# Kernel tuning notes

Measured on AMD Instinct MI355X. Metric: run time of the kernel, lower is better.

Reference implementation:

```python
import jax, jax.numpy as jnp
import numpy as np

B, NQ, NK = 4, 2048, 2048
D_MODEL, D_K, D_V, H = 1024, 1024, 1024, 16


def setup_inputs() -> dict:
    key = jax.random.key(0)
    ks = jax.random.split(key, 8)
    return {
        "queries": jax.random.normal(ks[0], (B, NQ, D_MODEL), dtype=jnp.float32),
        "keys": jax.random.normal(ks[1], (B, NK, D_MODEL), dtype=jnp.float32),
        "values": jax.random.normal(ks[2], (B, NK, D_MODEL), dtype=jnp.float32),
        # nn.Linear weights init.normal_(std=0.001); stored here in (in, out) layout
        "Wq": jax.random.normal(ks[3], (D_MODEL, D_K), dtype=jnp.float32) * 0.001,
        "Wk": jax.random.normal(ks[4], (D_MODEL, D_K), dtype=jnp.float32) * 0.001,
        "Wv": jax.random.normal(ks[5], (D_MODEL, D_V), dtype=jnp.float32) * 0.001,
        "Wo": jax.random.normal(ks[6], (D_V, D_MODEL), dtype=jnp.float32) * 0.001,
        "bo": jnp.zeros((D_MODEL,), dtype=jnp.float32),
    }


def reference(queries, keys, values, Wq, Wk, Wv, Wo, bo):
    b_s, nq, _ = queries.shape
    nk = keys.shape[1]
    hd_k = D_K // H  # per-head key dim
    hd_v = D_V // H  # per-head value dim
    # projections -> [b, h, n, hd]
    q = (queries @ Wq).reshape(b_s, nq, H, hd_k).transpose(0, 2, 1, 3)
    k = (keys @ Wk).reshape(b_s, nk, H, hd_k).transpose(0, 2, 1, 3)
    v = (values @ Wv).reshape(b_s, nk, H, hd_v).transpose(0, 2, 1, 3)
    # NOTE: original scales by sqrt(d_k) (full d_k), not per-head dim
    att = jnp.einsum("bhqd,bhkd->bhqk", q, k) / np.float32(np.sqrt(D_K))
    att = jax.nn.softmax(att, axis=-1)
    # dropout = identity (eval mode)
    out = jnp.einsum("bhqk,bhkd->bhqd", att, v)
    out = out.transpose(0, 2, 1, 3).reshape(b_s, nq, D_V)
    return out @ Wo + bo
```

## Files before the change

kernel.cpp:

```cpp
#include <hip/hip_runtime.h>


#define DM    1024
#define NSEQ  2048
#define HEADS 16
#define HD    64

typedef float floatx4 __attribute__((ext_vector_type(4)));
typedef short s16x4   __attribute__((ext_vector_type(4)));
typedef short s16x8   __attribute__((ext_vector_type(8)));
typedef unsigned int u32x4 __attribute__((ext_vector_type(4)));

static __device__ __forceinline__ floatx4 mfma_bf16(s16x8 a, s16x8 b, floatx4 c) {
  return __builtin_amdgcn_mfma_f32_16x16x32_bf16(a, b, c, 0, 0, 0);
}

static __device__ __forceinline__ void gload_lds16(const void* g, void* l) {
  __builtin_amdgcn_global_load_lds(
      (const __attribute__((address_space(1))) unsigned*)g,
      (__attribute__((address_space(3))) unsigned*)l, 16, 0, 0);
}

static __device__ __forceinline__ unsigned lds_addr(const void* p) {
  return (unsigned)(unsigned long long)p;
}

static __device__ __forceinline__ s16x8 ds_read_b128a(unsigned byteaddr) {
  s16x8 r;
  asm volatile("ds_read_b128 %0, %1" : "=v"(r) : "v"(byteaddr));
  return r;
}

#define WAIT_LGKM0() \
  { asm volatile("s_waitcnt lgkmcnt(0)" ::: "memory"); __builtin_amdgcn_sched_barrier(0); }

static __device__ __forceinline__ short f2bf(float f) {
  unsigned u = __builtin_bit_cast(unsigned, f);
  u += 0x7FFFu + ((u >> 16) & 1u);
  return (short)(u >> 16);
}

static __device__ __forceinline__ unsigned cvtpk_bf16(float lo, float hi) {
  unsigned r;
  asm("v_cvt_pk_bf16_f32 %0, %1, %2" : "=v"(r) : "v"(lo), "v"(hi));
  return r;
}

static __device__ __forceinline__ unsigned pack2_bf16(float a, float b) {
  unsigned ua = __builtin_bit_cast(unsigned, a) + 0x8000u;
  unsigned ub = __builtin_bit_cast(unsigned, b) + 0x8000u;
#if __has_builtin(__builtin_amdgcn_perm)
  return __builtin_amdgcn_perm(ub, ua, 0x07060302u);
#else
  return (ub & 0xffff0000u) | (ua >> 16);
#endif
}

__global__ __launch_bounds__(256) void make_wgroups(
    const float* __restrict__ W0, const float* __restrict__ W1,
    const float* __restrict__ W2, const float* __restrict__ W3,
    short* __restrict__ G0, short* __restrict__ G1,
    short* __restrict__ G2, short* __restrict__ G3) {
  __shared__ float tile[64][68];
  const int m = blockIdx.z;
  const float* W = m == 0 ? W0 : m == 1 ? W1 : m == 2 ? W2 : W3;
  short*       G = m == 0 ? G0 : m == 1 ? G1 : m == 2 ? G2 : G3;
  const int nt = blockIdx.x, kt = blockIdx.y;
  const int n0 = nt * 64, k0 = kt * 64;
  const int t = threadIdx.x;
  for (int j = 0; j < 4; j++) {
    int idx = j * 256 + t, r = idx >> 4, cq = idx & 15;
    *(floatx4*)&tile[r][cq * 4] = *(const floatx4*)(W + (long)(k0 + r) * DM + n0 + cq * 4);
  }
  __syncthreads();
  for (int j = 0; j < 2; j++) {
    int ci = j * 256 + t;
    int lm = ci & 15, quad = (ci >> 4) & 3, kk = (ci >> 6) & 1, gl = ci >> 7;
    s16x8 v;
#pragma unroll
    for (int e = 0; e < 8; e++) v[e] = f2bf(tile[kk * 32 + quad * 8 + e][gl * 16 + lm]);
    long addr;
    if (m < 3) {
      int ct = nt >> 2, g16 = (nt & 3) * 4 + gl;
      addr = ((long)(ct * 16 + kt)) * 16384 + (g16 * 2 + kk) * 512 + (quad * 16 + lm) * 8;
    } else {
      int ct = nt >> 1, g16 = (nt & 1) * 4 + gl;
      addr = ((long)(ct * 16 + kt)) * 8192 + (g16 * 2 + kk) * 512 + (quad * 16 + lm) * 8;
    }
    *(s16x8*)(G + addr) = v;
  }
}

__global__ __launch_bounds__(512, 2) void proj_kernel(
    const float* __restrict__ Aq, const float* __restrict__ Ak, const float* __restrict__ Av,
    const short* __restrict__ BgQ, const short* __restrict__ BgK, const short* __restrict__ BgV,
    short* __restrict__ Qh, short* __restrict__ KVg) {
  __shared__ short lds[2 * 24576];
  const int z = blockIdx.z;
  const float* A  = z == 0 ? Aq  : z == 1 ? Ak  : Av;
  const short* Bg = z == 0 ? BgQ : z == 1 ? BgK : BgV;
  const int t = threadIdx.x;
  const int w = t >> 6, l = t & 63, quad = l >> 4, lm = l & 15;
  const int wm = w >> 2, wn = w & 3;
  const int row0 = blockIdx.x * 128;
  const int ct = blockIdx.y;
  const int col0 = ct * 256;

  floatx4 acc[4][4];
  for (int mi = 0; mi < 4; mi++)
    for (int ni = 0; ni < 4; ni++) acc[mi][ni] = (floatx4){0.f, 0.f, 0.f, 0.f};

  floatx4 ar[2][2];
  auto loadA = [&](int ks) __attribute__((always_inline)) {
#pragma unroll
    for (int j = 0; j < 2; j++) {
      int tt = j * 512 + t, r = tt >> 3, c8 = (tt & 7) * 8;
      const float* p = A + (long)(row0 + r) * DM + ks * 64 + c8;
      ar[j][0] = *(const floatx4*)p;
      ar[j][1] = *(const floatx4*)(p + 4);
    }
  };
  auto writeA = [&](int buf) __attribute__((always_inline)) {
#pragma unroll
    for (int j = 0; j < 2; j++) {
      int tt = j * 512 + t, r = tt >> 3;
      int kk = (tt & 7) >> 2, q4 = tt & 3, lm2 = r & 15, g16 = r >> 4;
      u32x4 pk = {cvtpk_bf16(ar[j][0][0], ar[j][0][1]), cvtpk_bf16(ar[j][0][2], ar[j][0][3]),
                  cvtpk_bf16(ar[j][1][0], ar[j][1][1]), cvtpk_bf16(ar[j][1][2], ar[j][1][3])};
      int l3 = q4 * 16 + (lm2 ^ (q4 * 2));
      *(s16x8*)(lds + buf * 24576 + (g16 * 2 + kk) * 512 + l3 * 8) =
          __builtin_bit_cast(s16x8, pk);
    }
  };
  auto stageB = [&](int ks, int buf) __attribute__((always_inline)) {
#pragma unroll
    for (int i = 0; i < 4; i++) {
      int gb = w * 4 + i;
      const short* src = Bg + ((long)(ct * 16 + ks)) * 16384 + gb * 512 + l * 8;
      gload_lds16(src, lds + buf * 24576 + 8192 + gb * 512);
    }
  };

  const unsigned lds0 = lds_addr(lds);
  auto process = [&](int buf) __attribute__((always_inline)) {
    const unsigned lbase = lds0 + buf * 49152;
    const unsigned aswz = (quad * 16 + (lm ^ (quad * 2))) * 16;
#pragma unroll
    for (int kk = 0; kk < 2; kk++) {
      s16x8 af[4], bfr[4];
#pragma unroll
      for (int mi = 0; mi < 4; mi++)
        af[mi] = ds_read_b128a(lbase + ((wm * 4 + mi) * 2 + kk) * 1024 + aswz);
#pragma unroll
      for (int ni = 0; ni < 4; ni++)
        bfr[ni] = ds_read_b128a(lbase + 16384 + ((wn * 4 + ni) * 2 + kk) * 1024 + l * 16);
      WAIT_LGKM0();
      __builtin_amdgcn_s_setprio(1);
#pragma unroll
      for (int mi = 0; mi < 4; mi++)
#pragma unroll
        for (int ni = 0; ni < 4; ni++)
          acc[mi][ni] = mfma_bf16(af[mi], bfr[ni], acc[mi][ni]);
      __builtin_amdgcn_s_setprio(0);
    }
  };

  loadA(0);
  stageB(0, 0);
  writeA(0);
  __syncthreads();
  int cur = 0;
  for (int ks = 0; ks < 16; ++ks) {
    if (ks + 1 < 16) { loadA(ks + 1); stageB(ks + 1, cur ^ 1); }
    __builtin_amdgcn_sched_barrier(0);
    process(cur);
    if (ks + 1 < 16) writeA(cur ^ 1);
    __syncthreads();
    cur ^= 1;
  }

  const int rowbase = row0 + wm * 64;
  const int colbase = col0 + wn * 64;
  const int b = rowbase >> 11;
  const int h = colbase >> 6;
  const int rloc = rowbase & 2047;
  if (z == 0) {
    const float osc = 0.0450842200277801f;
    long base = ((long)(b * HEADS + h)) * NSEQ * HD;
    for (int mi = 0; mi < 4; mi++)
      for (int r = 0; r < 4; r++) {
        int q = rloc + mi * 16 + quad * 4 + r;
        long rowoff = base + (long)q * HD + lm;
        for (int ni = 0; ni < 4; ni++)
          Qh[rowoff + ni * 16] = f2bf(acc[mi][ni][r] * osc);
      }
  } else if (z == 1) {
    long bhb = ((long)(b * HEADS + h)) * 262144;
    for (int mi = 0; mi < 4; mi++)
      for (int r = 0; r < 4; r++) {
        int q = rloc + mi * 16 + quad * 4 + r;
        int tile = q >> 7, s = (q >> 5) & 3, jj = (q >> 4) & 1, lmk = q & 15;
        for (int ni = 0; ni < 4; ni++) {
          int c = ni >> 1, quadk = (ni * 2 + (lm >> 3)) & 3, ek = lm & 7;
          long addr = bhb + (long)tile * 16384 + (s * 4 + jj * 2 + c) * 512 +
                      (quadk * 16 + lmk) * 8 + ek;
          KVg[addr] = f2bf(acc[mi][ni][r]);
        }
      }
  } else {
    long bhb = ((long)(b * HEADS + h)) * 262144;
    for (int mi = 0; mi < 4; mi++)
      for (int r = 0; r < 4; r++) {
        int kc = rloc + (mi >> 1) * 32 + quad * 8 + (mi & 1) * 4 + r;
        int tile = kc >> 7, s = (kc >> 5) & 3, ev = (mi & 1) * 4 + r;
        for (int ni = 0; ni < 4; ni++) {
          long addr = bhb + (long)tile * 16384 + (16 + s * 4 + ni) * 512 +
                      (quad * 16 + lm) * 8 + ev;
          KVg[addr] = f2bf(acc[mi][ni][r]);
        }
      }
  }
}

__global__ __launch_bounds__(256, 2) void attn_kernel(
    const short* __restrict__ Qh, const short* __restrict__ KVg,
    short* __restrict__ Obf) {
  __shared__ short lds[2 * 16384];
  const int t = threadIdx.x;
  const int w = t >> 6, l = t & 63, quad = l >> 4, lm = l & 15;
  const int bh = blockIdx.x;
  const int qtile = blockIdx.y * 128 + w * 32;
  const short* Qp  = Qh  + (long)bh * NSEQ * HD;
  const short* KVp = KVg + (long)bh * 262144;

  s16x8 aq[2][2];
#pragma unroll
  for (int qi = 0; qi < 2; qi++)
#pragma unroll
    for (int c = 0; c < 2; c++)
      aq[qi][c] = *(const s16x8*)(Qp + (long)(qtile + qi * 16 + lm) * HD + c * 32 + quad * 8);

  floatx4 acc[2][4];
  float lsum[2] = {0.f, 0.f};
#pragma unroll
  for (int qi = 0; qi < 2; qi++)
#pragma unroll
    for (int n = 0; n < 4; n++) acc[qi][n] = (floatx4){0.f, 0.f, 0.f, 0.f};

  auto stage = [&](int kt, int buf) __attribute__((always_inline)) {
    short* base = lds + buf * 16384;
    const short* tsrc = KVp + (long)(kt >> 7) * 16384;
#pragma unroll
    for (int i = 0; i < 8; i++) {
      int g = w * 8 + i;
      gload_lds16(tsrc + g * 512 + l * 8, base + g * 512);
    }
  };

  auto process = [&](const short* Lb, int s) __attribute__((always_inline)) {
    s16x8 bk[2][2];
#pragma unroll
    for (int j = 0; j < 2; j++)
#pragma unroll
      for (int c = 0; c < 2; c++)
        bk[j][c] = *(const s16x8*)(Lb + ((s * 4 + j * 2 + c) * 64 + l) * 8);
    s16x8 vraw[4];
#pragma unroll
    for (int n = 0; n < 4; n++)
      vraw[n] = *(const s16x8*)(Lb + ((16 + s * 4 + n) * 64 + l) * 8);
#pragma unroll
    for (int qi = 0; qi < 2; qi++) {
      floatx4 sT[2];
      sT[0] = (floatx4){0.f, 0.f, 0.f, 0.f};
      sT[1] = (floatx4){0.f, 0.f, 0.f, 0.f};
      __builtin_amdgcn_s_setprio(1);
#pragma unroll
      for (int c = 0; c < 2; c++) {
        sT[0] = mfma_bf16(bk[0][c], aq[qi][c], sT[0]);
        sT[1] = mfma_bf16(bk[1][c], aq[qi][c], sT[1]);
      }
      __builtin_amdgcn_s_setprio(0);
      float p0 = __builtin_amdgcn_exp2f(sT[0][0]);
      float p1 = __builtin_amdgcn_exp2f(sT[0][1]);
      float p2 = __builtin_amdgcn_exp2f(sT[0][2]);
      float p3 = __builtin_amdgcn_exp2f(sT[0][3]);
      float p4 = __builtin_amdgcn_exp2f(sT[1][0]);
      float p5 = __builtin_amdgcn_exp2f(sT[1][1]);
      float p6 = __builtin_amdgcn_exp2f(sT[1][2]);
      float p7 = __builtin_amdgcn_exp2f(sT[1][3]);
      lsum[qi] += ((p0 + p1) + (p2 + p3)) + ((p4 + p5) + (p6 + p7));
      u32x4 pw = {pack2_bf16(p0, p1), pack2_bf16(p2, p3),
                  pack2_bf16(p4, p5), pack2_bf16(p6, p7)};
      s16x8 pcat = __builtin_bit_cast(s16x8, pw);
      __builtin_amdgcn_s_setprio(1);
#pragma unroll
      for (int n = 0; n < 4; n++)
        acc[qi][n] = mfma_bf16(vraw[n], pcat, acc[qi][n]);
      __builtin_amdgcn_s_setprio(0);
    }
  };

  stage(0, 0);
  __syncthreads();
  int cur = 0;
  for (int kt = 0; kt < NSEQ; kt += 128) {
    if (kt + 128 < NSEQ) stage(kt + 128, cur ^ 1);
    const short* Lb = lds + cur * 16384;
    process(Lb, 0);
    process(Lb, 1);
    process(Lb, 2);
    process(Lb, 3);
    __syncthreads();
    cur ^= 1;
  }

  const int b = bh >> 4, h = bh & 15;
  short* Ow = lds + w * 1152;
  const int erow = l >> 2, ecg = l & 3;
#pragma unroll
  for (int qi = 0; qi < 2; qi++) {
    float ls = lsum[qi];
    ls += __shfl_xor(ls, 16);
    ls += __shfl_xor(ls, 32);
    float rl = 1.0f / ls;
#pragma unroll
    for (int n = 0; n < 4; n++)
#pragma unroll
      for (int r = 0; r < 4; r++)
        Ow[lm * 72 + n * 16 + quad * 4 + r] = f2bf(acc[qi][n][r] * rl);
    s16x8 o0 = *(const s16x8*)(Ow + erow * 72 + ecg * 16);
    s16x8 o1 = *(const s16x8*)(Ow + erow * 72 + ecg * 16 + 8);
    long gaddr = ((long)(b * NSEQ + qtile + qi * 16 + erow)) * DM + h * HD + ecg * 16;
    *(s16x8*)(Obf + gaddr) = o0;
    *(s16x8*)(Obf + gaddr + 8) = o1;
  }
}

__global__ __launch_bounds__(256, 2) void out_kernel(
    const short* __restrict__ Ab, const short* __restrict__ WoG,
    const float* __restrict__ bias, float* __restrict__ Out) {
  __shared__ short lds[2 * 16384];
  const int t = threadIdx.x;
  const int w = t >> 6, l = t & 63, quad = l >> 4, lm = l & 15;
  const int wm = w >> 1, wn = w & 1;
  const int row0 = blockIdx.x * 128;
  const int ct = blockIdx.y;
  const int col0 = ct * 128;

  floatx4 acc[4][4];
  for (int mi = 0; mi < 4; mi++)
    for (int ni = 0; ni < 4; ni++) acc[mi][ni] = (floatx4){0.f, 0.f, 0.f, 0.f};

  s16x8 ar[4];
  auto loadA = [&](int ks) __attribute__((always_inline)) {
#pragma unroll
    for (int j = 0; j < 4; j++) {
      int tt = j * 256 + t, r = tt >> 3, c = tt & 7;
      ar[j] = *(const s16x8*)(Ab + (long)(row0 + r) * DM + ks * 64 + c * 8);
    }
  };
  auto writeA = [&](int buf) __attribute__((always_inline)) {
#pragma unroll
    for (int j = 0; j < 4; j++) {
      int tt = j * 256 + t, r = tt >> 3, c = tt & 7;
      int kk = c >> 2, q4 = c & 3, lm2 = r & 15, g16 = r >> 4;
      int l3 = q4 * 16 + (lm2 ^ (q4 * 2));
      *(s16x8*)(lds + buf * 16384 + (g16 * 2 + kk) * 512 + l3 * 8) = ar[j];
    }
  };
  auto stageB = [&](int ks, int buf) __attribute__((always_inline)) {
#pragma unroll
    for (int i = 0; i < 4; i++) {
      int gb = w * 4 + i;
      const short* src = WoG + ((long)(ct * 16 + ks)) * 8192 + gb * 512 + l * 8;
      gload_lds16(src, lds + buf * 16384 + 8192 + gb * 512);
    }
  };
  const unsigned lds0 = lds_addr(lds);
  auto process = [&](int buf) __attribute__((always_inline)) {
    const unsigned lbase = lds0 + buf * 32768;
    const unsigned aswz = (quad * 16 + (lm ^ (quad * 2))) * 16;
#pragma unroll
    for (int kk = 0; kk < 2; kk++) {
      s16x8 af[4], bfr[4];
#pragma unroll
      for (int mi = 0; mi < 4; mi++)
        af[mi] = ds_read_b128a(lbase + ((wm * 4 + mi) * 2 + kk) * 1024 + aswz);
#pragma unroll
      for (int ni = 0; ni < 4; ni++)
        bfr[ni] = ds_read_b128a(lbase + 16384 + ((wn * 4 + ni) * 2 + kk) * 1024 + l * 16);
      WAIT_LGKM0();
      __builtin_amdgcn_s_setprio(1);
#pragma unroll
      for (int mi = 0; mi < 4; mi++)
#pragma unroll
        for (int ni = 0; ni < 4; ni++)
          acc[mi][ni] = mfma_bf16(af[mi], bfr[ni], acc[mi][ni]);
      __builtin_amdgcn_s_setprio(0);
    }
  };

  loadA(0);
  stageB(0, 0);
  writeA(0);
  __syncthreads();
  int cur = 0;
  for (int ks = 0; ks < 16; ++ks) {
    if (ks + 1 < 16) { loadA(ks + 1); stageB(ks + 1, cur ^ 1); }
    __builtin_amdgcn_sched_barrier(0);
    process(cur);
    if (ks + 1 < 16) writeA(cur ^ 1);
    __syncthreads();
    cur ^= 1;
  }

  const int rowbase = row0 + wm * 64;
  const int colbase = col0 + wn * 64;
  for (int mi = 0; mi < 4; mi++)
    for (int r = 0; r < 4; r++) {
      int gr = rowbase + mi * 16 + quad * 4 + r;
      for (int ni = 0; ni < 4; ni++) {
        int gc = colbase + ni * 16 + lm;
        Out[(long)gr * DM + gc] = acc[mi][ni][r] + bias[gc];
      }
    }
}

extern "C" void kernel_launch(void* const* d_in, const int* in_sizes, int n_in,
                              void* d_out, int out_size, void* d_ws, size_t ws_size,
                              hipStream_t stream) {
  (void)in_sizes; (void)n_in; (void)out_size; (void)ws_size;
  const float* queries = (const float*)d_in[0];
  const float* keys    = (const float*)d_in[1];
  const float* values  = (const float*)d_in[2];
  const float* Wq = (const float*)d_in[3];
  const float* Wk = (const float*)d_in[4];
  const float* Wv = (const float*)d_in[5];
  const float* Wo = (const float*)d_in[6];
  const float* bo = (const float*)d_in[7];
  float* out = (float*)d_out;

  char* ws = (char*)d_ws;
  const size_t MB = 1024 * 1024;
  short* WqG = (short*)(ws + 0 * MB);
  short* WkG = (short*)(ws + 2 * MB);
  short* WvG = (short*)(ws + 4 * MB);
  short* WoG = (short*)(ws + 6 * MB);
  short* Qh  = (short*)(ws + 8 * MB);
  short* KVg = (short*)(ws + 24 * MB);
  short* Obf = (short*)(ws + 56 * MB);

  make_wgroups<<<dim3(16, 16, 4), 256, 0, stream>>>(
      Wq, Wk, Wv, Wo, WqG, WkG, WvG, WoG);
  proj_kernel<<<dim3(64, 4, 3), 512, 0, stream>>>(
      queries, keys, values, WqG, WkG, WvG, Qh, KVg);
  attn_kernel<<<dim3(64, 16), 256, 0, stream>>>(Qh, KVg, Obf);
  out_kernel<<<dim3(64, 8), 256, 0, stream>>>(Obf, WoG, bo, out);
}
```

Baseline: 318.5 us.

## Triple-buffer GEMM LDS stages and prefetch weight panels two steps ahead

The projection and output GEMM kernels move from double-buffered LDS to a three-slot ring. Weight tiles are staged via global_load_lds two iterations ahead, and explicit vmcnt/lgkmcnt waits with a raw s_barrier replace __syncthreads, so in-flight loads are not fully drained each step. The output GEMM also halves its K-step to 32, shrinking its LDS footprint while doubling the iteration count. The aim is to hide global load latency behind MFMA work. The cost is more LDS in the projection kernel and hand-tuned wait counts that must stay consistent with the number of issued loads.

```diff
diff --git a/kernel.cpp b/kernel.cpp
--- a/kernel.cpp
+++ b/kernel.cpp
@@ -31,8 +31,11 @@
   return r;
 }
 
+#define SCHED0() __builtin_amdgcn_sched_barrier(0)
 #define WAIT_LGKM0() \
   { asm volatile("s_waitcnt lgkmcnt(0)" ::: "memory"); __builtin_amdgcn_sched_barrier(0); }
+#define WAIT_VMCNT(N) \
+  { asm volatile("s_waitcnt vmcnt(" #N ")" ::: "memory"); __builtin_amdgcn_sched_barrier(0); }
 
 static __device__ __forceinline__ short f2bf(float f) {
   unsigned u = __builtin_bit_cast(unsigned, f);
@@ -95,7 +98,7 @@
     const float* __restrict__ Aq, const float* __restrict__ Ak, const float* __restrict__ Av,
     const short* __restrict__ BgQ, const short* __restrict__ BgK, const short* __restrict__ BgV,
     short* __restrict__ Qh, short* __restrict__ KVg) {
-  __shared__ short lds[2 * 24576];
+  __shared__ short lds[3 * 24576];
   const int z = blockIdx.z;
   const float* A  = z == 0 ? Aq  : z == 1 ? Ak  : Av;
   const short* Bg = z == 0 ? BgQ : z == 1 ? BgK : BgV;
@@ -133,17 +136,18 @@
     }
   };
   auto stageB = [&](int ks, int buf) __attribute__((always_inline)) {
+    const long pan = ((long)(ct * 16 + ks)) * 16384;
 #pragma unroll
     for (int i = 0; i < 4; i++) {
       int gb = w * 4 + i;
-      const short* src = Bg + ((long)(ct * 16 + ks)) * 16384 + gb * 512 + l * 8;
+      const short* src = Bg + pan + gb * 512 + l * 8;
       gload_lds16(src, lds + buf * 24576 + 8192 + gb * 512);
     }
   };
 
   const unsigned lds0 = lds_addr(lds);
   auto process = [&](int buf) __attribute__((always_inline)) {
-    const unsigned lbase = lds0 + buf * 49152;
+    const unsigned lbase = lds0 + buf * 49152u;
     const unsigned aswz = (quad * 16 + (lm ^ (quad * 2))) * 16;
 #pragma unroll
     for (int kk = 0; kk < 2; kk++) {
@@ -167,16 +171,21 @@
 
   loadA(0);
   stageB(0, 0);
+  stageB(1, 1);
   writeA(0);
-  __syncthreads();
-  int cur = 0;
+  WAIT_VMCNT(4);
+  WAIT_LGKM0();
+  __builtin_amdgcn_s_barrier();
+
   for (int ks = 0; ks < 16; ++ks) {
-    if (ks + 1 < 16) { loadA(ks + 1); stageB(ks + 1, cur ^ 1); }
-    __builtin_amdgcn_sched_barrier(0);
-    process(cur);
-    if (ks + 1 < 16) writeA(cur ^ 1);
-    __syncthreads();
-    cur ^= 1;
+    if (ks + 1 < 16) loadA(ks + 1);
+    if (ks + 2 < 16) stageB(ks + 2, (ks + 2) % 3);
+    SCHED0();
+    process(ks % 3);
+    if (ks + 1 < 16) writeA((ks + 1) % 3);
+    WAIT_VMCNT(4);
+    WAIT_LGKM0();
+    __builtin_amdgcn_s_barrier();
   }
 
   const int rowbase = row0 + wm * 64;
@@ -339,7 +348,7 @@
 __global__ __launch_bounds__(256, 2) void out_kernel(
     const short* __restrict__ Ab, const short* __restrict__ WoG,
     const float* __restrict__ bias, float* __restrict__ Out) {
-  __shared__ short lds[2 * 16384];
+  __shared__ short lds[3 * 8192];
   const int t = threadIdx.x;
   const int w = t >> 6, l = t & 63, quad = l >> 4, lm = l & 15;
   const int wm = w >> 1, wn = w & 1;
@@ -351,67 +360,71 @@
   for (int mi = 0; mi < 4; mi++)
     for (int ni = 0; ni < 4; ni++) acc[mi][ni] = (floatx4){0.f, 0.f, 0.f, 0.f};
 
-  s16x8 ar[4];
-  auto loadA = [&](int ks) __attribute__((always_inline)) {
-#pragma unroll
-    for (int j = 0; j < 4; j++) {
-      int tt = j * 256 + t, r = tt >> 3, c = tt & 7;
-      ar[j] = *(const s16x8*)(Ab + (long)(row0 + r) * DM + ks * 64 + c * 8);
+  s16x8 ar[2];
+  auto loadA = [&](int kt) __attribute__((always_inline)) {
+#pragma unroll
+    for (int j = 0; j < 2; j++) {
+      int tt = j * 256 + t, r = tt >> 2, c = tt & 3;
+      ar[j] = *(const s16x8*)(Ab + (long)(row0 + r) * DM + kt * 32 + c * 8);
     }
   };
   auto writeA = [&](int buf) __attribute__((always_inline)) {
 #pragma unroll
-    for (int j = 0; j < 4; j++) {
-      int tt = j * 256 + t, r = tt >> 3, c = tt & 7;
-      int kk = c >> 2, q4 = c & 3, lm2 = r & 15, g16 = r >> 4;
+    for (int j = 0; j < 2; j++) {
+      int tt = j * 256 + t, r = tt >> 2, q4 = tt & 3;
+      int lm2 = r & 15, g16 = r >> 4;
       int l3 = q4 * 16 + (lm2 ^ (q4 * 2));
-      *(s16x8*)(lds + buf * 16384 + (g16 * 2 + kk) * 512 + l3 * 8) = ar[j];
-    }
-  };
-  auto stageB = [&](int ks, int buf) __attribute__((always_inline)) {
-#pragma unroll
-    for (int i = 0; i < 4; i++) {
-      int gb = w * 4 + i;
-      const short* src = WoG + ((long)(ct * 16 + ks)) * 8192 + gb * 512 + l * 8;
-      gload_lds16(src, lds + buf * 16384 + 8192 + gb * 512);
+      *(s16x8*)(lds + buf * 8192 + g16 * 512 + l3 * 8) = ar[j];
+    }
+  };
+  auto stageB = [&](int kt, int buf) __attribute__((always_inline)) {
+    const long pan = ((long)(ct * 16 + (kt >> 1))) * 8192;
+    const int kk = kt & 1;
+#pragma unroll
+    for (int i = 0; i < 2; i++) {
+      int gb = w * 2 + i;
+      const short* src = WoG + pan + (gb * 2 + kk) * 512 + l * 8;
+      gload_lds16(src, lds + buf * 8192 + 4096 + gb * 512);
     }
   };
   const unsigned lds0 = lds_addr(lds);
   auto process = [&](int buf) __attribute__((always_inline)) {
-    const unsigned lbase = lds0 + buf * 32768;
+    const unsigned lbase = lds0 + buf * 16384;
     const unsigned aswz = (quad * 16 + (lm ^ (quad * 2))) * 16;
-#pragma unroll
-    for (int kk = 0; kk < 2; kk++) {
-      s16x8 af[4], bfr[4];
-#pragma unroll
-      for (int mi = 0; mi < 4; mi++)
-        af[mi] = ds_read_b128a(lbase + ((wm * 4 + mi) * 2 + kk) * 1024 + aswz);
+    s16x8 af[4], bfr[4];
+#pragma unroll
+    for (int mi = 0; mi < 4; mi++)
+      af[mi] = ds_read_b128a(lbase + (wm * 4 + mi) * 1024 + aswz);
+#pragma unroll
+    for (int ni = 0; ni < 4; ni++)
+      bfr[ni] = ds_read_b128a(lbase + 8192 + (wn * 4 + ni) * 1024 + l * 16);
+    WAIT_LGKM0();
+    __builtin_amdgcn_s_setprio(1);
+#pragma unroll
+    for (int mi = 0; mi < 4; mi++)
 #pragma unroll
       for (int ni = 0; ni < 4; ni++)
-        bfr[ni] = ds_read_b128a(lbase + 16384 + ((wn * 4 + ni) * 2 + kk) * 1024 + l * 16);
-      WAIT_LGKM0();
-      __builtin_amdgcn_s_setprio(1);
-#pragma unroll
-      for (int mi = 0; mi < 4; mi++)
-#pragma unroll
-        for (int ni = 0; ni < 4; ni++)
-          acc[mi][ni] = mfma_bf16(af[mi], bfr[ni], acc[mi][ni]);
-      __builtin_amdgcn_s_setprio(0);
-    }
+        acc[mi][ni] = mfma_bf16(af[mi], bfr[ni], acc[mi][ni]);
+    __builtin_amdgcn_s_setprio(0);
   };
 
   loadA(0);
   stageB(0, 0);
+  stageB(1, 1);
   writeA(0);
-  __syncthreads();
-  int cur = 0;
-  for (int ks = 0; ks < 16; ++ks) {
-    if (ks + 1 < 16) { loadA(ks + 1); stageB(ks + 1, cur ^ 1); }
-    __builtin_amdgcn_sched_barrier(0);
-    process(cur);
-    if (ks + 1 < 16) writeA(cur ^ 1);
-    __syncthreads();
-    cur ^= 1;
+  WAIT_VMCNT(2);
+  WAIT_LGKM0();
+  __builtin_amdgcn_s_barrier();
+
+  for (int kt = 0; kt < 32; ++kt) {
+    if (kt + 1 < 32) loadA(kt + 1);
+    if (kt + 2 < 32) stageB(kt + 2, (kt + 2) % 3);
+    SCHED0();
+    process(kt % 3);
+    if (kt + 1 < 32) writeA((kt + 1) % 3);
+    WAIT_VMCNT(2);
+    WAIT_LGKM0();
+    __builtin_amdgcn_s_barrier();
   }
 
   const int rowbase = row0 + wm * 64;
```

New measurement: 321.6 us. Within noise of the previous version (+1.0%).
